# Optimization experiments

Measured on AMD Instinct MI355X. Metric: run time of the kernel, lower is better.

The kernel has to match this reference:

```python
import jax, jax.numpy as jnp
import numpy as np

NEG_SLOPE = 0.2  # PyG GATConv default negative_slope


def _gat_conv(h, src, dst, N, W, a_src, a_dst, b, heads):
    """PyG GATConv (eval mode, self-loops already in src/dst).
    h: [N, F_in], W: [F_in, heads*C], a_src/a_dst: [heads, C], b: [heads*C]."""
    C = W.shape[1] // heads
    hl = (h @ W).reshape(N, heads, C)                      # [N,H,C]
    al_s = jnp.einsum('nhc,hc->nh', hl, a_src)             # [N,H]
    al_d = jnp.einsum('nhc,hc->nh', hl, a_dst)             # [N,H]
    e = jax.nn.leaky_relu(al_s[src] + al_d[dst], NEG_SLOPE)  # [E,H]
    # segment softmax over incoming edges of each destination node
    m = jax.ops.segment_max(e, dst, num_segments=N)        # [N,H]
    ex = jnp.exp(e - m[dst])
    s = jax.ops.segment_sum(ex, dst, num_segments=N)
    alpha = ex / (s[dst] + 1e-16)                          # [E,H]
    out = jax.ops.segment_sum(hl[src] * alpha[:, :, None], dst, num_segments=N)
    return out.reshape(N, heads * C) + b


def setup_inputs() -> dict:
    key = jax.random.key(0)
    ks = jax.random.split(key, 16)
    N, E, D = 30000, 240000, 64
    NUM_ENT, NUM_REL, NUM_DRUGS = 100000, 64, 200
    sc = 0.1
    return {
        'x': jax.random.randint(ks[0], (N,), 0, NUM_ENT),
        'edge_index': jax.random.randint(ks[1], (2, E), 0, N),
        'edge_type': jax.random.randint(ks[2], (N,), 0, NUM_REL),
        'ent_emb': jax.random.normal(ks[3], (NUM_ENT, D), jnp.float32) * sc,
        'rel_emb': jax.random.normal(ks[4], (NUM_REL, D), jnp.float32) * sc,
        'W1': jax.random.normal(ks[5], (2 * D, 8 * D), jnp.float32) * sc,
        'att1_src': jax.random.normal(ks[6], (8, D), jnp.float32) * sc,
        'att1_dst': jax.random.normal(ks[7], (8, D), jnp.float32) * sc,
        'b1': jax.random.normal(ks[8], (8 * D,), jnp.float32) * sc,
        'W2': jax.random.normal(ks[9], (9 * D, D), jnp.float32) * sc,
        'att2_src': jax.random.normal(ks[10], (1, D), jnp.float32) * sc,
        'att2_dst': jax.random.normal(ks[11], (1, D), jnp.float32) * sc,
        'b2': jax.random.normal(ks[12], (D,), jnp.float32) * sc,
        'fc_w': jax.random.normal(ks[13], (D, NUM_DRUGS), jnp.float32) * sc,
        'fc_b': jax.random.normal(ks[14], (NUM_DRUGS,), jnp.float32) * sc,
    }


def reference(x, edge_index, edge_type, ent_emb, rel_emb, W1, att1_src, att1_dst, b1,
              W2, att2_src, att2_dst, b2, fc_w, fc_b):
    N = x.shape[0]
    loop = jnp.arange(N)
    src = jnp.concatenate([edge_index[0], loop])  # GATConv add_self_loops=True
    dst = jnp.concatenate([edge_index[1], loop])
    ent = ent_emb[x]                               # [N,D]
    rel = rel_emb[edge_type]                       # [N,D]
    h = jnp.concatenate([ent, rel], axis=-1)       # [N,2D]  (dropout is identity in eval)
    h = jax.nn.elu(_gat_conv(h, src, dst, N, W1, att1_src, att1_dst, b1, heads=8))  # [N,8D]
    h = jnp.concatenate([h, ent], axis=-1)         # [N,9D]
    h = jax.nn.elu(_gat_conv(h, src, dst, N, W2, att2_src, att2_dst, b2, heads=1))  # [N,D]
    g = jnp.mean(h, axis=0, keepdims=True)         # [1,D]
    return g @ fc_w + fc_b                         # [1,num_drugs]
```

## Files before the change

kernel.cpp:

```cpp
#include <hip/hip_runtime.h>
#include <math.h>

#define NEG_SLOPE 0.2f

typedef __attribute__((ext_vector_type(8))) short short8;
typedef __attribute__((ext_vector_type(4))) float f32x4;
typedef __attribute__((ext_vector_type(2))) float f32x2;

__device__ __forceinline__ float lrelu(float v) { return v > 0.f ? v : NEG_SLOPE * v; }
__device__ __forceinline__ float elu(float v) { return v > 0.f ? v : (__expf(v) - 1.f); }
__device__ __forceinline__ unsigned short f2b(float f) {
    unsigned u = __float_as_uint(f);
    return (unsigned short)((u + 0x7FFFu + ((u >> 16) & 1u)) >> 16);
}
__device__ __forceinline__ unsigned packb(float a, float b) {
    return ((unsigned)f2b(b) << 16) | (unsigned)f2b(a);
}
__device__ __forceinline__ unsigned short pack8(float a, float b) {
    return (unsigned short)(__builtin_amdgcn_cvt_pk_fp8_f32(a, b, 0, false) & 0xFFFF);
}
__device__ __forceinline__ f32x2 unpack8(unsigned v) {
    return __builtin_amdgcn_cvt_pk_f32_fp8((int)v, false);
}
__device__ __forceinline__ f32x2 unpack8hi(unsigned v) {
    return __builtin_amdgcn_cvt_pk_f32_fp8((int)v, true);
}
__device__ __forceinline__ unsigned bpack_trunc(f32x2 f) {
    return (__float_as_uint(f.y) & 0xFFFF0000u) | (__float_as_uint(f.x) >> 16);
}
__device__ __forceinline__ int sw(int r, int o) { return (o ^ (r & 7)) << 3; }

__global__ void prep_k(const int* __restrict__ x, const int* __restrict__ et,
                       const int* __restrict__ ei,
                       const float* __restrict__ ent_emb, const float* __restrict__ rel_emb,
                       const float* __restrict__ W1, const float* __restrict__ W2,
                       unsigned* __restrict__ h1b2, unsigned short* __restrict__ W1t,
                       unsigned short* __restrict__ W2t, unsigned char* __restrict__ h2q8,
                       int* __restrict__ deg, int N, int E) {
    int t = blockIdx.x * blockDim.x + threadIdx.x;
    if (t < N * 64) {
        int n = t >> 6, j = t & 63;
        float v0, v1;
        if (j < 32) {
            const float* e = ent_emb + (size_t)x[n] * 64 + 2 * j;
            v0 = e[0]; v1 = e[1];
            *(unsigned short*)(h2q8 + (size_t)n * 576 + 512 + 2 * j) = pack8(v0, v1);
        } else {
            const float* r = rel_emb + (size_t)et[n] * 64 + 2 * (j - 32);
            v0 = r[0]; v1 = r[1];
        }
        h1b2[t] = packb(v0, v1);
    }
    if (t < 512 * 128) {
        int n = t >> 7, kk = t & 127;
        W1t[t] = f2b(W1[(size_t)kk * 512 + n]);
    }
    if (t < 64 * 576) {
        int n = t / 576, k = t % 576;
        W2t[t] = f2b(W2[(size_t)k * 64 + n]);
    }
    if (t < E + N) {
        int dst = t < E ? ei[E + t] : t - E;
        atomicAdd(&deg[dst], 1);
    }
}

__global__ __launch_bounds__(256) void scan_k(const int* __restrict__ deg,
                                              int* __restrict__ offs,
                                              int* __restrict__ bstate,
                                              int N, int Etot, int NB) {
    __shared__ int s[256];
    __shared__ int sbase;
    int b = blockIdx.x, t = threadIdx.x;
    int i = b * 256 + t;
    int v = (i < N) ? deg[i] : 0;
    s[t] = v;
    __syncthreads();
    for (int off = 1; off < 256; off <<= 1) {
        int tmp = (t >= off) ? s[t - off] : 0;
        __syncthreads();
        s[t] += tmp;
        __syncthreads();
    }
    int total = s[255];
    if (t == 0) {
        if (b == 0) {
            atomicExch(&bstate[0], (total << 2) | 2);
            sbase = 0;
        } else {
            atomicExch(&bstate[b], (total << 2) | 1);
            int run = 0;
            for (int p = b - 1; p >= 0;) {
                int stv;
                do { stv = atomicAdd(&bstate[p], 0); } while ((stv & 3) == 0);
                run += (stv >> 2);
                if ((stv & 3) == 2) break;
                p--;
            }
            atomicExch(&bstate[b], ((run + total) << 2) | 2);
            sbase = run;
        }
    }
    __syncthreads();
    if (i < N) offs[i] = sbase + s[t] - v;
    if (b == NB - 1 && t == 0) offs[N] = Etot;
}

__global__ __launch_bounds__(256) void fillgemm1_k(const int* __restrict__ ei, int E, int N,
                                                   const int* __restrict__ offs,
                                                   int* __restrict__ cursor,
                                                   int* __restrict__ csr,
                                                   const unsigned short* __restrict__ A,
                                                   const unsigned short* __restrict__ W1t,
                                                   const float* __restrict__ a1s,
                                                   const float* __restrict__ a1d,
                                                   unsigned char* __restrict__ hl8,
                                                   float* __restrict__ als,
                                                   float* __restrict__ ald,
                                                   int FB, int NMB) {
    __shared__ __align__(16) unsigned char Cs[128 * 64];
    int bid = blockIdx.x;
    int tid = threadIdx.x;
    if (bid < FB) {
        int e = bid * 256 + tid;
        if (e < E + N) {
            int src = e < E ? ei[e] : e - E;
            int dst = e < E ? ei[E + e] : e - E;
            int pos = offs[dst] + atomicAdd(&cursor[dst], 1);
            csr[pos] = src;
        }
        return;
    }
    int g = bid - FB;
    int h = g / NMB, mb = g - h * NMB;
    int m0 = mb * 128;
    int M = N;
    int w = tid >> 6, lane = tid & 63;
    int wr = w * 32;
    int m16 = lane & 15, quad = lane >> 4;
    f32x4 acc[2][4] = {};
#pragma unroll
    for (int kk = 0; kk < 128; kk += 32) {
        int col = kk + quad * 8;
        short8 b[4];
#pragma unroll
        for (int j = 0; j < 4; j++)
            b[j] = *(const short8*)(W1t + (size_t)(h * 64 + j * 16 + m16) * 128 + col);
#pragma unroll
        for (int i = 0; i < 2; i++) {
            int r = m0 + wr + i * 16 + m16;
            short8 a = {};
            if (r < M) a = *(const short8*)(A + (size_t)r * 128 + col);
#pragma unroll
            for (int j = 0; j < 4; j++)
                acc[i][j] = __builtin_amdgcn_mfma_f32_16x16x32_bf16(a, b[j], acc[i][j], 0, 0, 0);
        }
    }
    float sa[2][4] = {}, sd[2][4] = {};
#pragma unroll
    for (int j = 0; j < 4; j++) {
        int col = h * 64 + j * 16 + m16;
        float ws_ = a1s[col], wd_ = a1d[col];
#pragma unroll
        for (int i = 0; i < 2; i++)
#pragma unroll
            for (int reg = 0; reg < 4; reg++) {
                sa[i][reg] += acc[i][j][reg] * ws_;
                sd[i][reg] += acc[i][j][reg] * wd_;
            }
    }
#pragma unroll
    for (int m = 1; m < 16; m <<= 1)
#pragma unroll
        for (int i = 0; i < 2; i++)
#pragma unroll
            for (int reg = 0; reg < 4; reg++) {
                sa[i][reg] += __shfl_xor(sa[i][reg], m, 64);
                sd[i][reg] += __shfl_xor(sd[i][reg], m, 64);
            }
    if (m16 == 0)
#pragma unroll
        for (int i = 0; i < 2; i++)
#pragma unroll
            for (int reg = 0; reg < 4; reg++) {
                int row = m0 + wr + i * 16 + quad * 4 + reg;
                if (row < M) { als[row * 8 + h] = sa[i][reg]; ald[row * 8 + h] = sd[i][reg]; }
            }
#pragma unroll
    for (int i = 0; i < 2; i++)
#pragma unroll
        for (int j = 0; j < 4; j++)
#pragma unroll
            for (int reg = 0; reg < 4; reg++) {
                int lr = wr + i * 16 + quad * 4 + reg;
                Cs[lr * 64 + j * 16 + m16] =
                    (unsigned char)(__builtin_amdgcn_cvt_pk_fp8_f32(acc[i][j][reg] * 8.f,
                                                                    0.f, 0, false) & 0xFF);
            }
    __syncthreads();
    for (int c = tid; c < 512; c += 256) {
        int row = c >> 2, off = c & 3;
        int grow = m0 + row;
        if (grow < M)
            *(uint4*)(hl8 + (size_t)grow * 512 + h * 64 + off * 16) =
                *(const uint4*)(Cs + c * 16);
    }
}

#define ACCP(e_, u_)                                      \
    {                                                     \
        f32x2 g0 = unpack8(u_.x), g1 = unpack8hi(u_.x);   \
        f32x2 g2 = unpack8(u_.y), g3 = unpack8hi(u_.y);   \
        acc[0] += (e_) * g0.x; acc[1] += (e_) * g0.y;     \
        acc[2] += (e_) * g1.x; acc[3] += (e_) * g1.y;     \
        acc[4] += (e_) * g2.x; acc[5] += (e_) * g2.y;     \
        acc[6] += (e_) * g3.x; acc[7] += (e_) * g3.y;     \
    }

__global__ __launch_bounds__(256) void agg1_k(const unsigned char* __restrict__ hl8,
                                              const float* __restrict__ als1,
                                              const float* __restrict__ ald1,
                                              const float* __restrict__ b1,
                                              const int* __restrict__ offs,
                                              const int* __restrict__ csr,
                                              unsigned char* __restrict__ h2q8, int N) {
    int wv = threadIdx.x >> 6;
    int t = threadIdx.x & 63;
    int n = blockIdx.x * 4 + wv;
    if (n >= N) return;
    int h = t >> 3;
    float dl = ald1[n * 8 + h];
    int p0 = offs[n], p1 = offs[n + 1];
    float acc[8] = {};
    float ssum = 0.f;
    int p = p0;
    for (; p + 4 <= p1; p += 4) {
        int sA = csr[p], sB = csr[p + 1], sC = csr[p + 2], sD = csr[p + 3];
        float eA = __expf(lrelu(als1[sA * 8 + h] + dl));
        float eB = __expf(lrelu(als1[sB * 8 + h] + dl));
        float eC = __expf(lrelu(als1[sC * 8 + h] + dl));
        float eD = __expf(lrelu(als1[sD * 8 + h] + dl));
        uint2 vA = *(const uint2*)(hl8 + (size_t)sA * 512 + t * 8);
        uint2 vB = *(const uint2*)(hl8 + (size_t)sB * 512 + t * 8);
        uint2 vC = *(const uint2*)(hl8 + (size_t)sC * 512 + t * 8);
        uint2 vD = *(const uint2*)(hl8 + (size_t)sD * 512 + t * 8);
        ssum += (eA + eB) + (eC + eD);
        ACCP(eA, vA);
        ACCP(eB, vB);
        ACCP(eC, vC);
        ACCP(eD, vD);
    }
    for (; p < p1; p++) {
        int sA = csr[p];
        float eA = __expf(lrelu(als1[sA * 8 + h] + dl));
        uint2 vA = *(const uint2*)(hl8 + (size_t)sA * 512 + t * 8);
        ssum += eA;
        ACCP(eA, vA);
    }
    float iv = 0.125f / (ssum + 1e-16f);
    float4 bq0 = *(const float4*)(b1 + t * 8);
    float4 bq1 = *(const float4*)(b1 + t * 8 + 4);
    float r0 = elu(acc[0] * iv + bq0.x);
    float r1 = elu(acc[1] * iv + bq0.y);
    float r2 = elu(acc[2] * iv + bq0.z);
    float r3 = elu(acc[3] * iv + bq0.w);
    float r4 = elu(acc[4] * iv + bq1.x);
    float r5 = elu(acc[5] * iv + bq1.y);
    float r6 = elu(acc[6] * iv + bq1.z);
    float r7 = elu(acc[7] * iv + bq1.w);
    uint2 o;
    int d0 = __builtin_amdgcn_cvt_pk_fp8_f32(r0, r1, 0, false);
    o.x = (unsigned)__builtin_amdgcn_cvt_pk_fp8_f32(r2, r3, d0, true);
    int d1 = __builtin_amdgcn_cvt_pk_fp8_f32(r4, r5, 0, false);
    o.y = (unsigned)__builtin_amdgcn_cvt_pk_fp8_f32(r6, r7, d1, true);
    *(uint2*)(h2q8 + (size_t)n * 576 + t * 8) = o;
}

__global__ __launch_bounds__(256) void gemm2_k(const unsigned char* __restrict__ Aq8,
                                               const unsigned short* __restrict__ Bt,
                                               const float* __restrict__ a2s,
                                               const float* __restrict__ a2d,
                                               unsigned char* __restrict__ hl2q,
                                               float* __restrict__ als2,
                                               float* __restrict__ ald2, int M) {
    __shared__ __align__(16) unsigned short As[64 * 64];
    __shared__ __align__(16) unsigned short Bs[64 * 64];
    int tid = threadIdx.x;
    int m0 = blockIdx.x * 64;
    int w = tid >> 6, lane = tid & 63;
    int m16 = lane & 15, quad = lane >> 4;
    f32x4 acc[4] = {};
    for (int k0 = 0; k0 < 576; k0 += 64) {
        __syncthreads();
        {
            int r = tid >> 2, o = tid & 3;
            int gr = m0 + r;
            uint4 v = make_uint4(0u, 0u, 0u, 0u);
            if (gr < M) v = *(const uint4*)(Aq8 + (size_t)gr * 576 + k0 + o * 16);
            uint4 w0, w1;
            w0.x = bpack_trunc(unpack8(v.x));   w0.y = bpack_trunc(unpack8hi(v.x));
            w0.z = bpack_trunc(unpack8(v.y));   w0.w = bpack_trunc(unpack8hi(v.y));
            w1.x = bpack_trunc(unpack8(v.z));   w1.y = bpack_trunc(unpack8hi(v.z));
            w1.z = bpack_trunc(unpack8(v.w));   w1.w = bpack_trunc(unpack8hi(v.w));
            *(uint4*)(As + r * 64 + sw(r, 2 * o)) = w0;
            *(uint4*)(As + r * 64 + sw(r, 2 * o + 1)) = w1;
        }
        for (int c = tid; c < 512; c += 256) {
            int r = c >> 3, o = c & 7;
            uint4 v = *(const uint4*)(Bt + (size_t)r * 576 + k0 + o * 8);
            *(uint4*)(Bs + r * 64 + sw(r, o)) = v;
        }
        __syncthreads();
#pragma unroll
        for (int kk = 0; kk < 64; kk += 32) {
            int ob = (kk >> 3) + quad;
            int r = w * 16 + m16;
            short8 a = *(const short8*)(As + r * 64 + sw(r, ob));
#pragma unroll
            for (int j = 0; j < 4; j++) {
                int rb = j * 16 + m16;
                short8 b = *(const short8*)(Bs + rb * 64 + sw(rb, ob));
                acc[j] = __builtin_amdgcn_mfma_f32_16x16x32_bf16(a, b, acc[j], 0, 0, 0);
            }
        }
    }
#pragma unroll
    for (int j = 0; j < 4; j++)
#pragma unroll
        for (int reg = 0; reg < 4; reg++) {
            int row = m0 + w * 16 + quad * 4 + reg;
            int col = j * 16 + m16;
            if (row < M)
                hl2q[(size_t)row * 64 + col] =
                    (unsigned char)(__builtin_amdgcn_cvt_pk_fp8_f32(acc[j][reg], 0.f, 0, false) & 0xFF);
        }
    float sa[4] = {}, sd[4] = {};
#pragma unroll
    for (int j = 0; j < 4; j++) {
        int col = j * 16 + m16;
        float as_ = a2s[col], ad_ = a2d[col];
#pragma unroll
        for (int reg = 0; reg < 4; reg++) {
            sa[reg] += acc[j][reg] * as_;
            sd[reg] += acc[j][reg] * ad_;
        }
    }
#pragma unroll
    for (int m = 1; m < 16; m <<= 1)
#pragma unroll
        for (int reg = 0; reg < 4; reg++) {
            sa[reg] += __shfl_xor(sa[reg], m, 64);
            sd[reg] += __shfl_xor(sd[reg], m, 64);
        }
    if (m16 == 0)
#pragma unroll
        for (int reg = 0; reg < 4; reg++) {
            int row = m0 + w * 16 + quad * 4 + reg;
            if (row < M) { als2[row] = sa[reg]; ald2[row] = sd[reg]; }
        }
}

__global__ __launch_bounds__(256) void agg2_k(const unsigned short* __restrict__ hl2q16,
                                              const float* __restrict__ als2,
                                              const float* __restrict__ ald2,
                                              const float* __restrict__ b2,
                                              const int* __restrict__ offs,
                                              const int* __restrict__ csr,
                                              float* __restrict__ gpart, int N) {
    __shared__ float red[512];
    int slot = threadIdx.x >> 5, l = threadIdx.x & 31;
    int n = blockIdx.x * 8 + slot;
    float v0 = 0.f, v1 = 0.f;
    if (n < N) {
        float dl = ald2[n];
        int p0 = offs[n], p1 = offs[n + 1];
        float a0 = 0.f, a1 = 0.f, ssum = 0.f;
        int p = p0;
        for (; p + 1 < p1; p += 2) {
            int sA = csr[p], sB = csr[p + 1];
            float lA = als2[sA], lB = als2[sB];
            unsigned hA = hl2q16[sA * 32 + l];
            unsigned hB = hl2q16[sB * 32 + l];
            float xA = __expf(lrelu(lA + dl));
            float xB = __expf(lrelu(lB + dl));
            ssum += xA + xB;
            f32x2 fA = unpack8(hA), fB = unpack8(hB);
            a0 += xA * fA.x + xB * fB.x;
            a1 += xA * fA.y + xB * fB.y;
        }
        if (p < p1) {
            int sA = csr[p];
            float xA = __expf(lrelu(als2[sA] + dl));
            ssum += xA;
            f32x2 fA = unpack8(hl2q16[sA * 32 + l]);
            a0 += xA * fA.x;
            a1 += xA * fA.y;
        }
        float inv = 1.f / (ssum + 1e-16f);
        v0 = elu(a0 * inv + b2[2 * l]);
        v1 = elu(a1 * inv + b2[2 * l + 1]);
    }
    red[slot * 64 + 2 * l] = v0;
    red[slot * 64 + 2 * l + 1] = v1;
    __syncthreads();
    if (threadIdx.x < 64) {
        float s = 0.f;
#pragma unroll
        for (int ss = 0; ss < 8; ss++) s += red[ss * 64 + threadIdx.x];
        gpart[(size_t)blockIdx.x * 64 + threadIdx.x] = s;
    }
}

__global__ __launch_bounds__(256) void colredfinal_k(const float* __restrict__ gpart,
                                                     float* __restrict__ gsum,
                                                     int* __restrict__ done,
                                                     const float* __restrict__ fcw,
                                                     const float* __restrict__ fcb,
                                                     float* __restrict__ out,
                                                     int NBL, int N, int NCB) {
    __shared__ float red[256];
    __shared__ int isLast;
    int t = threadIdx.x;
    int c = t & 63, rg = t >> 6;
    int bend = blockIdx.x * 256 + 256; if (bend > NBL) bend = NBL;
    float acc = 0.f;
    for (int b = blockIdx.x * 256 + rg; b < bend; b += 4)
        acc += gpart[(size_t)b * 64 + c];
    red[t] = acc;
    __syncthreads();
    if (t < 64) atomicAdd(&gsum[c], red[c] + red[c + 64] + red[c + 128] + red[c + 192]);
    __threadfence();
    if (t == 0) {
        int old = atomicAdd(done, 1);
        isLast = (old == NCB - 1) ? 1 : 0;
    }
    __syncthreads();
    if (isLast) {
        __shared__ float g[64];
        if (t < 64) g[t] = atomicAdd(&gsum[t], 0.f) / (float)N;
        __syncthreads();
        if (t < 200) {
            float a = fcb[t];
#pragma unroll
            for (int cc = 0; cc < 64; cc++) a += g[cc] * fcw[cc * 200 + t];
            out[t] = a;
        }
    }
}

extern "C" void kernel_launch(void* const* d_in, const int* in_sizes, int n_in,
                              void* d_out, int out_size, void* d_ws, size_t ws_size,
                              hipStream_t stream) {
    const int* x = (const int*)d_in[0];
    const int* ei = (const int*)d_in[1];
    const int* et = (const int*)d_in[2];
    const float* ent_emb = (const float*)d_in[3];
    const float* rel_emb = (const float*)d_in[4];
    const float* W1 = (const float*)d_in[5];
    const float* a1s = (const float*)d_in[6];
    const float* a1d = (const float*)d_in[7];
    const float* b1 = (const float*)d_in[8];
    const float* W2 = (const float*)d_in[9];
    const float* a2s = (const float*)d_in[10];
    const float* a2d = (const float*)d_in[11];
    const float* b2 = (const float*)d_in[12];
    const float* fcw = (const float*)d_in[13];
    const float* fcb = (const float*)d_in[14];
    float* out = (float*)d_out;

    int N = in_sizes[0];
    int E = in_sizes[1] / 2;
    int Etot = E + N;
    int NB = (N + 255) / 256;
    int NBL = (N + 7) / 8;
    int NCB = (NBL + 255) / 256;
    int FB = (Etot + 255) / 256;
    int NMB = (N + 127) / 128;

    char* p = (char*)d_ws;
    auto alloc = [&](size_t bytes) -> char* {
        char* r = p;
        p += (bytes + 255) & ~(size_t)255;
        return r;
    };
    unsigned* h1b2 = (unsigned*)alloc((size_t)N * 64 * 4);
    unsigned short* W1t = (unsigned short*)alloc((size_t)512 * 128 * 2);
    unsigned short* W2t = (unsigned short*)alloc((size_t)64 * 576 * 2);
    float* als1 = (float*)alloc((size_t)N * 8 * 4);
    float* ald1 = (float*)alloc((size_t)N * 8 * 4);
    unsigned char* hl8 = (unsigned char*)alloc((size_t)N * 512);
    unsigned char* h2q8 = (unsigned char*)alloc((size_t)N * 576);
    unsigned char* hl2q = (unsigned char*)alloc((size_t)N * 64);
    float* als2 = (float*)alloc((size_t)N * 4);
    float* ald2 = (float*)alloc((size_t)N * 4);
    float* gpart = (float*)alloc((size_t)NBL * 64 * 4);
    int* offs   = (int*)alloc((size_t)(N + 1) * 4);
    int* csr    = (int*)alloc((size_t)Etot * 4);
    char* z0 = p;
    int* deg    = (int*)alloc((size_t)N * 4);
    int* cursor = (int*)alloc((size_t)N * 4);
    float* gsum = (float*)alloc(64 * 4);
    int* done   = (int*)alloc(4);
    int* bstate = (int*)alloc((size_t)NB * 4);
    size_t zbytes = (size_t)(p - z0);

    int tb = 256;
    hipMemsetAsync(z0, 0, zbytes, stream);
    prep_k<<<(N * 64 + tb - 1) / tb, tb, 0, stream>>>(x, et, ei, ent_emb, rel_emb,
                                                      W1, W2, h1b2, W1t, W2t, h2q8, deg, N, E);
    scan_k<<<NB, 256, 0, stream>>>(deg, offs, bstate, N, Etot, NB);
    fillgemm1_k<<<FB + NMB * 8, 256, 0, stream>>>(ei, E, N, offs, cursor, csr,
                                                  (const unsigned short*)h1b2, W1t,
                                                  a1s, a1d, hl8, als1, ald1, FB, NMB);
    agg1_k<<<(N + 3) / 4, 256, 0, stream>>>(hl8, als1, ald1, b1, offs, csr, h2q8, N);
    gemm2_k<<<(N + 63) / 64, 256, 0, stream>>>(h2q8, W2t, a2s, a2d, hl2q, als2, ald2, N);
    agg2_k<<<NBL, 256, 0, stream>>>((const unsigned short*)hl2q, als2, ald2, b2, offs, csr, gpart, N);
    colredfinal_k<<<NCB, 256, 0, stream>>>(gpart, gsum, done, fcw, fcb, out, NBL, N, NCB);
}
```

Measured before the change: 238.4 us.

## Split prep into role-specific blocks, tile weight transposes, and drop LDS staging in gemm2

prep_k is split into block ranges by role: embedding gather, degree counting, and weight transposes. The W1 and W2 transposes now go through a padded shared-memory tile so both the reads and the writes are coalesced, where the old strided per-thread reads were not. gemm2_k loads its fp8 A operand and bf16 B operand straight from global memory into registers, removing the LDS staging and the syncthreads inside the K loop. Its fp8 output is staged in shared memory so rows can be written with 16-byte stores. The trade-off is that B is re-read from global or L2 by every wave without LDS reuse, and the prep grid becomes larger.

```diff
diff --git a/kernel.cpp b/kernel.cpp
--- a/kernel.cpp
+++ b/kernel.cpp
@@ -30,38 +30,68 @@
 }
 __device__ __forceinline__ int sw(int r, int o) { return (o ^ (r & 7)) << 3; }
 
-__global__ void prep_k(const int* __restrict__ x, const int* __restrict__ et,
-                       const int* __restrict__ ei,
+__global__ __launch_bounds__(256) void prep_k(const int* __restrict__ x,
+                       const int* __restrict__ et, const int* __restrict__ ei,
                        const float* __restrict__ ent_emb, const float* __restrict__ rel_emb,
                        const float* __restrict__ W1, const float* __restrict__ W2,
                        unsigned* __restrict__ h1b2, unsigned short* __restrict__ W1t,
                        unsigned short* __restrict__ W2t, unsigned char* __restrict__ h2q8,
-                       int* __restrict__ deg, int N, int E) {
-    int t = blockIdx.x * blockDim.x + threadIdx.x;
-    if (t < N * 64) {
-        int n = t >> 6, j = t & 63;
-        float v0, v1;
-        if (j < 32) {
-            const float* e = ent_emb + (size_t)x[n] * 64 + 2 * j;
-            v0 = e[0]; v1 = e[1];
-            *(unsigned short*)(h2q8 + (size_t)n * 576 + 512 + 2 * j) = pack8(v0, v1);
-        } else {
-            const float* r = rel_emb + (size_t)et[n] * 64 + 2 * (j - 32);
-            v0 = r[0]; v1 = r[1];
-        }
-        h1b2[t] = packb(v0, v1);
-    }
-    if (t < 512 * 128) {
-        int n = t >> 7, kk = t & 127;
-        W1t[t] = f2b(W1[(size_t)kk * 512 + n]);
-    }
-    if (t < 64 * 576) {
-        int n = t / 576, k = t % 576;
-        W2t[t] = f2b(W2[(size_t)k * 64 + n]);
-    }
-    if (t < E + N) {
-        int dst = t < E ? ei[E + t] : t - E;
-        atomicAdd(&deg[dst], 1);
+                       int* __restrict__ deg, int N, int E, int NH1, int DEGB) {
+    __shared__ float T[64 * 65];
+    int bid = blockIdx.x, tid = threadIdx.x;
+    if (bid < NH1) {
+        int t = bid * 256 + tid;
+        if (t < N * 64) {
+            int n = t >> 6, j = t & 63;
+            float v0, v1;
+            if (j < 32) {
+                const float* e = ent_emb + (size_t)x[n] * 64 + 2 * j;
+                v0 = e[0]; v1 = e[1];
+                *(unsigned short*)(h2q8 + (size_t)n * 576 + 512 + 2 * j) = pack8(v0, v1);
+            } else {
+                const float* r = rel_emb + (size_t)et[n] * 64 + 2 * (j - 32);
+                v0 = r[0]; v1 = r[1];
+            }
+            h1b2[t] = packb(v0, v1);
+        }
+        return;
+    }
+    bid -= NH1;
+    if (bid < DEGB) {
+        int e = bid * 256 + tid;
+        if (e < E + N) {
+            int dst = e < E ? ei[E + e] : e - E;
+            atomicAdd(&deg[dst], 1);
+        }
+        return;
+    }
+    bid -= DEGB;
+    if (bid < 16) {
+        int kt = bid >> 3, nt = bid & 7;
+        for (int c = tid; c < 4096; c += 256) {
+            int r = c >> 6, o = c & 63;
+            T[o * 65 + r] = W1[(size_t)(kt * 64 + r) * 512 + nt * 64 + o];
+        }
+        __syncthreads();
+        for (int c = tid; c < 4096; c += 256) {
+            int n = c >> 6, k = c & 63;
+            W1t[(size_t)(nt * 64 + n) * 128 + kt * 64 + k] = f2b(T[n * 65 + k]);
+        }
+        return;
+    }
+    bid -= 16;
+    if (bid < 9) {
+        int kt = bid;
+        for (int c = tid; c < 4096; c += 256) {
+            int r = c >> 6, o = c & 63;
+            T[o * 65 + r] = W2[(size_t)(kt * 64 + r) * 64 + o];
+        }
+        __syncthreads();
+        for (int c = tid; c < 4096; c += 256) {
+            int n = c >> 6, k = c & 63;
+            W2t[(size_t)n * 576 + kt * 64 + k] = f2b(T[n * 65 + k]);
+        }
+        return;
     }
 }
 
@@ -283,57 +313,31 @@
                                                unsigned char* __restrict__ hl2q,
                                                float* __restrict__ als2,
                                                float* __restrict__ ald2, int M) {
-    __shared__ __align__(16) unsigned short As[64 * 64];
-    __shared__ __align__(16) unsigned short Bs[64 * 64];
+    __shared__ __align__(16) unsigned char Cs[64 * 64];
     int tid = threadIdx.x;
     int m0 = blockIdx.x * 64;
     int w = tid >> 6, lane = tid & 63;
     int m16 = lane & 15, quad = lane >> 4;
+    int arow = m0 + w * 16 + m16;
+    const unsigned char* ap = Aq8 + (size_t)arow * 576 + quad * 8;
+    bool aval = arow < M;
     f32x4 acc[4] = {};
-    for (int k0 = 0; k0 < 576; k0 += 64) {
-        __syncthreads();
-        {
-            int r = tid >> 2, o = tid & 3;
-            int gr = m0 + r;
-            uint4 v = make_uint4(0u, 0u, 0u, 0u);
-            if (gr < M) v = *(const uint4*)(Aq8 + (size_t)gr * 576 + k0 + o * 16);
-            uint4 w0, w1;
-            w0.x = bpack_trunc(unpack8(v.x));   w0.y = bpack_trunc(unpack8hi(v.x));
-            w0.z = bpack_trunc(unpack8(v.y));   w0.w = bpack_trunc(unpack8hi(v.y));
-            w1.x = bpack_trunc(unpack8(v.z));   w1.y = bpack_trunc(unpack8hi(v.z));
-            w1.z = bpack_trunc(unpack8(v.w));   w1.w = bpack_trunc(unpack8hi(v.w));
-            *(uint4*)(As + r * 64 + sw(r, 2 * o)) = w0;
-            *(uint4*)(As + r * 64 + sw(r, 2 * o + 1)) = w1;
-        }
-        for (int c = tid; c < 512; c += 256) {
-            int r = c >> 3, o = c & 7;
-            uint4 v = *(const uint4*)(Bt + (size_t)r * 576 + k0 + o * 8);
-            *(uint4*)(Bs + r * 64 + sw(r, o)) = v;
-        }
-        __syncthreads();
-#pragma unroll
-        for (int kk = 0; kk < 64; kk += 32) {
-            int ob = (kk >> 3) + quad;
-            int r = w * 16 + m16;
-            short8 a = *(const short8*)(As + r * 64 + sw(r, ob));
-#pragma unroll
-            for (int j = 0; j < 4; j++) {
-                int rb = j * 16 + m16;
-                short8 b = *(const short8*)(Bs + rb * 64 + sw(rb, ob));
-                acc[j] = __builtin_amdgcn_mfma_f32_16x16x32_bf16(a, b, acc[j], 0, 0, 0);
-            }
-        }
-    }
-#pragma unroll
-    for (int j = 0; j < 4; j++)
-#pragma unroll
-        for (int reg = 0; reg < 4; reg++) {
-            int row = m0 + w * 16 + quad * 4 + reg;
-            int col = j * 16 + m16;
-            if (row < M)
-                hl2q[(size_t)row * 64 + col] =
-                    (unsigned char)(__builtin_amdgcn_cvt_pk_fp8_f32(acc[j][reg], 0.f, 0, false) & 0xFF);
-        }
+#pragma unroll
+    for (int kk = 0; kk < 576; kk += 32) {
+        uint2 av = make_uint2(0u, 0u);
+        if (aval) av = *(const uint2*)(ap + kk);
+        uint4 aw;
+        aw.x = bpack_trunc(unpack8(av.x));
+        aw.y = bpack_trunc(unpack8hi(av.x));
+        aw.z = bpack_trunc(unpack8(av.y));
+        aw.w = bpack_trunc(unpack8hi(av.y));
+        short8 a = *(short8*)&aw;
+#pragma unroll
+        for (int j = 0; j < 4; j++) {
+            short8 b = *(const short8*)(Bt + (size_t)(j * 16 + m16) * 576 + kk + quad * 8);
+            acc[j] = __builtin_amdgcn_mfma_f32_16x16x32_bf16(a, b, acc[j], 0, 0, 0);
+        }
+    }
     float sa[4] = {}, sd[4] = {};
 #pragma unroll
     for (int j = 0; j < 4; j++) {
@@ -358,6 +362,21 @@
             int row = m0 + w * 16 + quad * 4 + reg;
             if (row < M) { als2[row] = sa[reg]; ald2[row] = sd[reg]; }
         }
+#pragma unroll
+    for (int j = 0; j < 4; j++)
+#pragma unroll
+        for (int reg = 0; reg < 4; reg++) {
+            int lr = w * 16 + quad * 4 + reg;
+            Cs[lr * 64 + j * 16 + m16] =
+                (unsigned char)(__builtin_amdgcn_cvt_pk_fp8_f32(acc[j][reg], 0.f, 0, false) & 0xFF);
+        }
+    __syncthreads();
+    if (tid < 256) {
+        int row = tid >> 2, off = tid & 3;
+        int grow = m0 + row;
+        if (grow < M)
+            *(uint4*)(hl2q + (size_t)grow * 64 + off * 16) = *(const uint4*)(Cs + tid * 16);
+    }
 }
 
 __global__ __launch_bounds__(256) void agg2_k(const unsigned short* __restrict__ hl2q16,
@@ -476,6 +495,8 @@
     int NCB = (NBL + 255) / 256;
     int FB = (Etot + 255) / 256;
     int NMB = (N + 127) / 128;
+    int NH1 = (N * 64 + 255) / 256;
+    int DEGB = (Etot + 255) / 256;
 
     char* p = (char*)d_ws;
     auto alloc = [&](size_t bytes) -> char* {
@@ -504,10 +525,10 @@
     int* bstate = (int*)alloc((size_t)NB * 4);
     size_t zbytes = (size_t)(p - z0);
 
-    int tb = 256;
     hipMemsetAsync(z0, 0, zbytes, stream);
-    prep_k<<<(N * 64 + tb - 1) / tb, tb, 0, stream>>>(x, et, ei, ent_emb, rel_emb,
-                                                      W1, W2, h1b2, W1t, W2t, h2q8, deg, N, E);
+    prep_k<<<NH1 + DEGB + 25, 256, 0, stream>>>(x, et, ei, ent_emb, rel_emb,
+                                                W1, W2, h1b2, W1t, W2t, h2q8, deg,
+                                                N, E, NH1, DEGB);
     scan_k<<<NB, 256, 0, stream>>>(deg, offs, bstate, N, Etot, NB);
     fillgemm1_k<<<FB + NMB * 8, 256, 0, stream>>>(ei, E, N, offs, cursor, csr,
                                                   (const unsigned short*)h1b2, W1t,
```

Measured after the change: 249.3 us. 1.05x slower.
